# Optimization experiments

Measured on AMD Instinct MI355X. Metric: run time of the kernel, lower is better.

The kernel has to match this reference:

```python
import jax, jax.numpy as jnp
import numpy as np

K = 16
REP = 128
ASZ = 6
AENC = 64
BSK = 2048 * K  # bs*K flat batch


def _lin(k, fin, fout):
    return jax.random.normal(k, (fin, fout), jnp.float32) / np.float32(np.sqrt(fin))


def setup_inputs() -> dict:
    key = jax.random.key(0)
    ks = jax.random.split(key, 20)
    inp = {
        "lambda1": jax.random.normal(ks[0], (BSK, REP), jnp.float32),
        "actions": jax.random.normal(ks[1], (BSK, ASZ), jnp.float32),
    }
    # (fan_in, hidden, fan_out) per rlkit Mlp((hidden,), out, in)
    specs = {
        "le": (REP, REP, REP),            # lambda_encoder
        "ae": (ASZ, REP, AENC),           # action_encoder
        "aef": (AENC + REP, REP, REP),    # action_effect_network
        "aat": (AENC + REP, REP, 1),      # action_attention_network
        "pe": (2 * REP, 2 * REP, REP),    # pairwise_encoder_network
        "ie": (REP, REP, AENC),           # interaction_effect_network
        "ia": (REP, REP, 1),              # interaction_attention_network
        "fm": (AENC + REP, REP, REP),     # final_merge_network
    }
    i = 2
    for name, (fin, h, fout) in specs.items():
        inp[name + "_W1"] = _lin(ks[i], fin, h)
        inp[name + "_b1"] = jnp.zeros((h,), jnp.float32)
        inp[name + "_W2"] = _lin(ks[i + 1], h, fout)
        inp[name + "_b2"] = jnp.zeros((fout,), jnp.float32)
        i += 2
    return inp


def _mlp(x, W1, b1, W2, b2, out_act):
    h = jax.nn.elu(x @ W1 + b1)
    return out_act(h @ W2 + b2)


# constant all-pairs index lists (i != j), i-major as in the torch loop
_II = np.array([i for i in range(K) for j in range(K) if i != j])
_JJ = np.array([j for i in range(K) for j in range(K) if i != j])


def reference(lambda1, actions,
              le_W1, le_b1, le_W2, le_b2,
              ae_W1, ae_b1, ae_W2, ae_b2,
              aef_W1, aef_b1, aef_W2, aef_b2,
              aat_W1, aat_b1, aat_W2, aat_b2,
              pe_W1, pe_b1, pe_W2, pe_b2,
              ie_W1, ie_b1, ie_W2, ie_b2,
              ia_W1, ia_b1, ia_W2, ia_b2,
              fm_W1, fm_b1, fm_W2, fm_b2):
    elu, sig = jax.nn.elu, jax.nn.sigmoid
    ident = lambda z: z

    enc_flat = _mlp(lambda1, le_W1, le_b1, le_W2, le_b2, elu)        # (BSK, REP)
    a_enc = _mlp(actions, ae_W1, ae_b1, ae_W2, ae_b2, elu)           # (BSK, AENC)
    la = jnp.concatenate([enc_flat, a_enc], -1)                      # (BSK, REP+AENC)
    a_eff = _mlp(la, aef_W1, aef_b1, aef_W2, aef_b2, elu)            # (BSK, REP)
    a_att = _mlp(la, aat_W1, aat_b1, aat_W2, aat_b2, sig)            # (BSK, 1)
    enc = (a_eff * a_att).reshape(-1, K, REP)                        # (bs, K, REP)
    bs = enc.shape[0]

    # all ordered pairs (i, j), i != j -> concat sender/receiver states
    all_pairs = jnp.concatenate([enc[:, _II], enc[:, _JJ]], -1)      # (bs, K*(K-1), 2*REP)
    all_pairs = all_pairs.reshape(bs * K, K - 1, 2 * REP)

    pi = _mlp(all_pairs, pe_W1, pe_b1, pe_W2, pe_b2, elu)            # (bs*K, K-1, REP)
    effect = _mlp(pi, ie_W1, ie_b1, ie_W2, ie_b2, elu)               # (bs*K, K-1, AENC)
    attention = _mlp(pi, ia_W1, ia_b1, ia_W2, ia_b2, sig)            # (bs*K, K-1, 1)
    total_effect = (effect * attention).sum(1)                       # (bs*K, AENC)

    lam_eff = jnp.concatenate([enc_flat, total_effect], -1)          # (bs*K, REP+AENC)
    new_lambdas = _mlp(lam_eff, fm_W1, fm_b1, fm_W2, fm_b2, ident)   # (bs*K, REP)
    return new_lambdas
```

## Files before the change

kernel.cpp:

```cpp
#include <hip/hip_runtime.h>
#include <hip/hip_bf16.h>

typedef unsigned short ushort_t;
typedef unsigned int uint_t;
typedef short bf16x8 __attribute__((ext_vector_type(8)));
typedef float f32x4 __attribute__((ext_vector_type(4)));

#define MFMA16(a, b, c) __builtin_amdgcn_mfma_f32_16x16x32_bf16((a), (b), (c), 0, 0, 0)

__device__ __forceinline__ ushort_t f2bf(float f) {
  uint_t u = __float_as_uint(f);
  u += 0x7fffu + ((u >> 16) & 1u);
  return (ushort_t)(u >> 16);
}
__device__ __forceinline__ float bf2f(ushort_t h) {
  return __uint_as_float(((uint_t)h) << 16);
}
__device__ __forceinline__ uint_t pack2(float lo, float hi) {
  union { __hip_bfloat162 h; uint_t u; } cv;
  cv.h = __float22bfloat162_rn(float2{lo, hi});
  return cv.u;
}
__device__ __forceinline__ uint2 pack4(f32x4 v) {
  uint2 o;
  o.x = pack2(v[0], v[1]);
  o.y = pack2(v[2], v[3]);
  return o;
}
__device__ __forceinline__ float eluf(float x) {
  float e = __expf(x) - 1.0f;
  return x > 0.0f ? x : e;
}
__device__ __forceinline__ float sigmf(float x) {
  return 1.0f / (1.0f + __expf(-x));
}
__device__ __forceinline__ int lds_off(int row, int colb, int ccb) {
  return row * ccb + (colb ^ ((row & 7) << 4));
}

constexpr size_t OFF_ENCF = 0;
constexpr size_t OFF_ENC  = 4194304;
constexpr size_t OFF_TEFF = 8388608;
constexpr size_t OFF_FR   = 10485760;
constexpr size_t OFF_U    = 10772480;
constexpr size_t OFF_V    = 19161088;

constexpr int FR_LE_W1  = 0;
constexpr int FR_LE_W2  = 16384;
constexpr int FR_AE_W2  = 32768;
constexpr int FR_AEF_W1 = 40960;
constexpr int FR_AAT_W1 = 65536;
constexpr int FR_AEF_W2 = 90112;
constexpr int FR_PE_W1  = 106496;
constexpr int FR_PE_W2  = 172032;
constexpr int FR_IE_W1  = 204800;
constexpr int FR_IE_W2  = 221184;
constexpr int FR_IA_W1  = 229376;
constexpr int FR_FM_W1  = 245760;
constexpr int FR_FM_W2  = 270336;

struct PrepDesc { const float* src; ushort_t* dst; int K; int N; };
struct PrepArgs { PrepDesc d[13]; };

__global__ __launch_bounds__(256) void prep_kernel(PrepArgs a) {
  PrepDesc p = a.d[blockIdx.y];
  int idx = blockIdx.x * 256 + threadIdx.x;
  if (idx >= p.K * p.N) return;
  int e = idx & 7;
  int lane = (idx >> 3) & 63;
  int f = idx >> 9;
  int ksteps = p.K >> 5;
  int kstep = f % ksteps;
  int ntile = f / ksteps;
  int k = kstep * 32 + ((lane >> 4) << 3) + e;
  int n = ntile * 16 + (lane & 15);
  p.dst[idx] = f2bf(p.src[k * p.N + n]);
}


template <int MT, int NT, int KS, int KSTR = KS>
__device__ __forceinline__ void reg_gemm_t(const bf16x8 x[MT][KS],
                                           const ushort_t* __restrict__ wfrag,
                                           int ntile0, int lane, f32x4 acc[MT][NT]) {
  const f32x4 z = {0.f, 0.f, 0.f, 0.f};
#pragma unroll
  for (int nt = 0; nt < NT; ++nt) {
#pragma unroll
    for (int m = 0; m < MT; ++m) acc[m][nt] = z;
    const ushort_t* wf = wfrag + (size_t)((ntile0 + nt) * KSTR) * 512 + lane * 8;
#pragma unroll
    for (int ks = 0; ks < KS; ++ks) {
      bf16x8 wfr = *(const bf16x8*)(wf + ks * 512);
#pragma unroll
      for (int m = 0; m < MT; ++m) acc[m][nt] = MFMA16(wfr, x[m][ks], acc[m][nt]);
    }
  }
}

template <int MT, int KS>
__device__ __forceinline__ void lds_load_x(const ushort_t* __restrict__ Abase, int lane,
                                           bf16x8 x[MT][KS]) {
  const int r = lane & 15, q = lane >> 4;
#pragma unroll
  for (int m = 0; m < MT; ++m)
#pragma unroll
    for (int ks = 0; ks < KS; ++ks) {
      int row = m * 16 + r;
      x[m][ks] = *(const bf16x8*)((const char*)Abase + lds_off(row, ks * 64 + q * 16, KS * 64));
    }
}

template <int MT, int NT, int KS>
__device__ __forceinline__ void lds_gemm_t(const ushort_t* __restrict__ Abase,
                                           const ushort_t* __restrict__ wfrag,
                                           int ntile0, int lane, f32x4 acc[MT][NT]) {
  bf16x8 x[MT][KS];
  lds_load_x<MT, KS>(Abase, lane, x);
  reg_gemm_t<MT, NT, KS>(x, wfrag, ntile0, lane, acc);
}

template <int MT, int NT, bool ELU>
__device__ __forceinline__ void add_bias_act_t(f32x4 acc[MT][NT], const float* __restrict__ bias,
                                               int col0, int lane) {
  const int q = lane >> 4;
#pragma unroll
  for (int nt = 0; nt < NT; ++nt) {
    f32x4 bv = *(const f32x4*)(bias + col0 + nt * 16 + q * 4);
#pragma unroll
    for (int m = 0; m < MT; ++m)
#pragma unroll
      for (int k = 0; k < 4; ++k) {
        float v = acc[m][nt][k] + bv[k];
        acc[m][nt][k] = ELU ? eluf(v) : v;
      }
  }
}

template <int MT, int NT, int CCB>
__device__ __forceinline__ void store_lds_t(ushort_t* Dbase, int col0, int lane,
                                            const f32x4 acc[MT][NT]) {
  const int r = lane & 15, q = lane >> 4;
#pragma unroll
  for (int m = 0; m < MT; ++m) {
    const int row = m * 16 + r;
#pragma unroll
    for (int nt = 0; nt < NT; ++nt) {
      int colb = (col0 + nt * 16 + q * 4) * 2;
      *(uint2*)((char*)Dbase + lds_off(row, colb, CCB)) = pack4(acc[m][nt]);
    }
  }
}

template <int MT, int NT>
__device__ __forceinline__ void store_global_t(ushort_t* __restrict__ G, int row0, int ncols,
                                               int col0, int lane, const f32x4 acc[MT][NT]) {
  const int r = lane & 15, q = lane >> 4;
#pragma unroll
  for (int m = 0; m < MT; ++m)
#pragma unroll
    for (int nt = 0; nt < NT; ++nt)
      *(uint2*)(G + (size_t)(row0 + m * 16 + r) * ncols + col0 + nt * 16 + q * 4) =
          pack4(acc[m][nt]);
}

__global__ __launch_bounds__(256, 2) void enc_kernel(
    const float* __restrict__ lambda1, const float* __restrict__ actions,
    const float* __restrict__ le_b1, const float* __restrict__ le_b2,
    const float* __restrict__ ae_W1, const float* __restrict__ ae_b1,
    const float* __restrict__ ae_b2, const float* __restrict__ aef_b1,
    const float* __restrict__ aef_b2, const float* __restrict__ aat_b1,
    const float* __restrict__ aat_W2, const float* __restrict__ aat_b2,
    const ushort_t* __restrict__ fr, ushort_t* __restrict__ encf, ushort_t* __restrict__ enc) {
  __shared__ __align__(16) ushort_t bufA[64 * 128];
  __shared__ __align__(16) ushort_t bufB[64 * 128];
  __shared__ __align__(16) ushort_t la[64 * 192];
  __shared__ float att[64];

  const int t = threadIdx.x, lane = t & 63, w = t >> 6;
  const int r = lane & 15, q = lane >> 4;
  const int rows0 = blockIdx.x * 64;

  {
    const int row = t >> 2, c0 = (t & 3) * 32;
    const float4* src = (const float4*)(lambda1 + (size_t)(rows0 + row) * 128 + c0);
#pragma unroll
    for (int j = 0; j < 8; ++j) {
      float4 v = src[j];
      f32x4 vv = {v.x, v.y, v.z, v.w};
      *(uint2*)((char*)bufA + lds_off(row, (c0 + j * 4) * 2, 256)) = pack4(vv);
    }
  }
  __syncthreads();

  f32x4 acc2[4][2];
  lds_gemm_t<4, 2, 4>(bufA, fr + FR_LE_W1, w * 2, lane, acc2);
  add_bias_act_t<4, 2, true>(acc2, le_b1, w * 32, lane);
  store_lds_t<4, 2, 256>(bufB, w * 32, lane, acc2);
  __syncthreads();
  lds_gemm_t<4, 2, 4>(bufB, fr + FR_LE_W2, w * 2, lane, acc2);
  add_bias_act_t<4, 2, true>(acc2, le_b2, w * 32, lane);
  store_lds_t<4, 2, 384>(la, w * 32, lane, acc2);
  store_global_t<4, 2>(encf, rows0, 128, w * 32, lane, acc2);
  {
    const int row = t >> 2, c0 = (t & 3) * 32;
    float a6[6];
#pragma unroll
    for (int k2 = 0; k2 < 6; ++k2) a6[k2] = actions[(size_t)(rows0 + row) * 6 + k2];
#pragma unroll
    for (int j = 0; j < 16; ++j) {
      int c = c0 + j * 2;
      float s0 = ae_b1[c], s1 = ae_b1[c + 1];
#pragma unroll
      for (int k2 = 0; k2 < 6; ++k2) {
        s0 += a6[k2] * ae_W1[k2 * 128 + c];
        s1 += a6[k2] * ae_W1[k2 * 128 + c + 1];
      }
      *(uint_t*)((char*)bufA + lds_off(row, c * 2, 256)) = pack2(eluf(s0), eluf(s1));
    }
  }
  __syncthreads();
  {
    f32x4 acc1[4][1];
    lds_gemm_t<4, 1, 4>(bufA, fr + FR_AE_W2, w, lane, acc1);
    add_bias_act_t<4, 1, true>(acc1, ae_b2, w * 16, lane);
    store_lds_t<4, 1, 384>(la, 128 + w * 16, lane, acc1);
  }
  __syncthreads();
  {
    bf16x8 xla[4][6];
    lds_load_x<4, 6>(la, lane, xla);
    reg_gemm_t<4, 2, 6>(xla, fr + FR_AEF_W1, w * 2, lane, acc2);
    add_bias_act_t<4, 2, true>(acc2, aef_b1, w * 32, lane);
    store_lds_t<4, 2, 256>(bufA, w * 32, lane, acc2);
    reg_gemm_t<4, 2, 6>(xla, fr + FR_AAT_W1, w * 2, lane, acc2);
    add_bias_act_t<4, 2, true>(acc2, aat_b1, w * 32, lane);
    store_lds_t<4, 2, 256>(bufB, w * 32, lane, acc2);
  }
  __syncthreads();
  lds_gemm_t<4, 2, 4>(bufA, fr + FR_AEF_W2, w * 2, lane, acc2);
  add_bias_act_t<4, 2, true>(acc2, aef_b2, w * 32, lane);
  {
    const int row = t >> 2, s = t & 3;
    float sum = 0.f;
#pragma unroll
    for (int j = 0; j < 32; ++j) {
      int c = s * 32 + j;
      sum += bf2f(*(const ushort_t*)((const char*)bufB + lds_off(row, c * 2, 256))) * aat_W2[c];
    }
    sum += __shfl_xor(sum, 1);
    sum += __shfl_xor(sum, 2);
    if (s == 0) att[row] = sigmf(sum + aat_b2[0]);
  }
  __syncthreads();
#pragma unroll
  for (int mt = 0; mt < 4; ++mt) {
    float av = att[mt * 16 + r];
#pragma unroll
    for (int nt = 0; nt < 2; ++nt) {
      f32x4 sv = acc2[mt][nt];
      sv[0] *= av; sv[1] *= av; sv[2] *= av; sv[3] *= av;
      *(uint2*)(enc + (size_t)(rows0 + mt * 16 + r) * 128 + w * 32 + nt * 16 + q * 4) = pack4(sv);
    }
  }
}

__global__ __launch_bounds__(256, 2) void uv_kernel(const ushort_t* __restrict__ enc,
                                                    const ushort_t* __restrict__ fr,
                                                    ushort_t* __restrict__ U,
                                                    ushort_t* __restrict__ V) {
  const int t = threadIdx.x, lane = t & 63, w = t >> 6;
  const int r = lane & 15, q = lane >> 4;
  const int rows0 = blockIdx.x * 64;
  const int half = blockIdx.y;

  bf16x8 x[4][4];
#pragma unroll
  for (int m = 0; m < 4; ++m)
#pragma unroll
    for (int ks = 0; ks < 4; ++ks)
      x[m][ks] = *(const bf16x8*)(enc + (size_t)(rows0 + m * 16 + r) * 128 + ks * 32 + q * 8);

  f32x4 acc[4][4];
  reg_gemm_t<4, 4, 4, 8>(x, fr + FR_PE_W1 + half * 4 * 512, w * 4, lane, acc);
  store_global_t<4, 4>(half ? V : U, rows0, 256, w * 64, lane, acc);
}

__global__ __launch_bounds__(256, 4) void pair_kernel(
    const ushort_t* __restrict__ U, const ushort_t* __restrict__ V,
    const ushort_t* __restrict__ fr,
    const float* __restrict__ pe_b1, const float* __restrict__ pe_b2,
    const float* __restrict__ ie_b1, const float* __restrict__ ie_b2,
    const float* __restrict__ ia_b1, const float* __restrict__ ia_W2,
    const float* __restrict__ ia_b2, ushort_t* __restrict__ teff) {
  __shared__ __align__(16) ushort_t hid[32 * 256];
  __shared__ __align__(16) ushort_t bufPi[32 * 128];
  __shared__ float att[32];

  const int t = threadIdx.x, lane = t & 63, w = t >> 6;
  const int r = lane & 15, q = lane >> 4;
  const int orig = ((blockIdx.x & 7) << 11) + (blockIdx.x >> 3);
  const int g0 = orig * 2;
  const int b = g0 >> 4;

  {
    const int token = t >> 3, c0 = (t & 7) * 32;
    const int im = (g0 + (token >> 4)) & 15;
    const ushort_t* Ur = U + (size_t)(b * 16 + im) * 256 + c0;
    const ushort_t* Vr = V + (size_t)(b * 16 + (token & 15)) * 256 + c0;
    const float* bp = pe_b1 + c0;
#pragma unroll
    for (int j4 = 0; j4 < 4; ++j4) {
      bf16x8 uu = *(const bf16x8*)(Ur + j4 * 8);
      bf16x8 vv = *(const bf16x8*)(Vr + j4 * 8);
      f32x4 b0 = *(const f32x4*)(bp + j4 * 8);
      f32x4 b1 = *(const f32x4*)(bp + j4 * 8 + 4);
      float h[8];
#pragma unroll
      for (int e = 0; e < 8; ++e) {
        float bb = (e < 4) ? b0[e] : b1[e - 4];
        h[e] = eluf(bf2f((ushort_t)uu[e]) + bf2f((ushort_t)vv[e]) + bb);
      }
      uint4 pk;
      pk.x = pack2(h[0], h[1]); pk.y = pack2(h[2], h[3]);
      pk.z = pack2(h[4], h[5]); pk.w = pack2(h[6], h[7]);
      *(uint4*)((char*)hid + lds_off(token, (c0 + j4 * 8) * 2, 512)) = pk;
    }
  }
  __syncthreads();
  {
    f32x4 acc[2][2];
    lds_gemm_t<2, 2, 8>(hid, fr + FR_PE_W2, w * 2, lane, acc);
    add_bias_act_t<2, 2, true>(acc, pe_b2, w * 32, lane);
    store_lds_t<2, 2, 256>(bufPi, w * 32, lane, acc);
  }
  __syncthreads();
  {
    bf16x8 x2[2][4];
    lds_load_x<2, 4>(bufPi, lane, x2);
    f32x4 acc[2][2];
    reg_gemm_t<2, 2, 4>(x2, fr + FR_IE_W1, w * 2, lane, acc);
    add_bias_act_t<2, 2, true>(acc, ie_b1, w * 32, lane);
    store_lds_t<2, 2, 256>(hid, w * 32, lane, acc);
    reg_gemm_t<2, 2, 4>(x2, fr + FR_IA_W1, w * 2, lane, acc);
    add_bias_act_t<2, 2, true>(acc, ia_b1, w * 32, lane);
    store_lds_t<2, 2, 256>(hid + 32 * 128, w * 32, lane, acc);
  }
  __syncthreads();
  f32x4 eff[2][1];
  lds_gemm_t<2, 1, 4>(hid, fr + FR_IE_W2, w, lane, eff);
  add_bias_act_t<2, 1, true>(eff, ie_b2, w * 16, lane);
  {
    const int row = t >> 3, s = t & 7;
    const char* hia = (const char*)(hid + 32 * 128);
    float sum = 0.f;
#pragma unroll
    for (int j = 0; j < 16; ++j) {
      int c = s * 16 + j;
      sum += bf2f(*(const ushort_t*)(hia + lds_off(row, c * 2, 256))) * ia_W2[c];
    }
    sum += __shfl_xor(sum, 1);
    sum += __shfl_xor(sum, 2);
    sum += __shfl_xor(sum, 4);
    if (s == 0) att[row] = sigmf(sum + ia_b2[0]);
  }
  __syncthreads();
#pragma unroll
  for (int mt = 0; mt < 2; ++mt) {
    const int im = (g0 + mt) & 15;
    const float av = (r == im) ? 0.f : att[mt * 16 + r];
    float v0 = eff[mt][0][0] * av, v1 = eff[mt][0][1] * av;
    float v2 = eff[mt][0][2] * av, v3 = eff[mt][0][3] * av;
#pragma unroll
    for (int d = 1; d < 16; d <<= 1) {
      v0 += __shfl_xor(v0, d);
      v1 += __shfl_xor(v1, d);
      v2 += __shfl_xor(v2, d);
      v3 += __shfl_xor(v3, d);
    }
    if (r == 0) {
      uint2 p;
      p.x = pack2(v0, v1);
      p.y = pack2(v2, v3);
      *(uint2*)(teff + (size_t)(g0 + mt) * 64 + w * 16 + q * 4) = p;
    }
  }
}

__global__ __launch_bounds__(256, 2) void fm_kernel(
    const ushort_t* __restrict__ encf, const ushort_t* __restrict__ teff,
    const ushort_t* __restrict__ fr, const float* __restrict__ fm_b1,
    const float* __restrict__ fm_b2, float* __restrict__ out) {
  __shared__ __align__(16) ushort_t bufH[64 * 128];
  const int t = threadIdx.x, lane = t & 63, w = t >> 6;
  const int r = lane & 15, q = lane >> 4;
  const int rows0 = blockIdx.x * 64;

  bf16x8 x[4][6];
#pragma unroll
  for (int mt = 0; mt < 4; ++mt) {
    const size_t row = rows0 + mt * 16 + r;
#pragma unroll
    for (int ks = 0; ks < 6; ++ks) {
      x[mt][ks] = (ks < 4) ? *(const bf16x8*)(encf + row * 128 + ks * 32 + q * 8)
                           : *(const bf16x8*)(teff + row * 64 + (ks - 4) * 32 + q * 8);
    }
  }
  f32x4 acc[4][2];
  reg_gemm_t<4, 2, 6>(x, fr + FR_FM_W1, w * 2, lane, acc);
  add_bias_act_t<4, 2, true>(acc, fm_b1, w * 32, lane);
  store_lds_t<4, 2, 256>(bufH, w * 32, lane, acc);
  __syncthreads();
  lds_gemm_t<4, 2, 4>(bufH, fr + FR_FM_W2, w * 2, lane, acc);
  add_bias_act_t<4, 2, false>(acc, fm_b2, w * 32, lane);
#pragma unroll
  for (int mt = 0; mt < 4; ++mt)
#pragma unroll
    for (int nt = 0; nt < 2; ++nt)
      *(f32x4*)(out + (size_t)(rows0 + mt * 16 + r) * 128 + w * 32 + nt * 16 + q * 4) =
          acc[mt][nt];
}

extern "C" void kernel_launch(void* const* d_in, const int* in_sizes, int n_in,
                              void* d_out, int out_size, void* d_ws, size_t ws_size,
                              hipStream_t stream) {
  (void)in_sizes; (void)n_in; (void)out_size; (void)ws_size;
  const float* lambda1 = (const float*)d_in[0];
  const float* actions = (const float*)d_in[1];

  ushort_t* ws = (ushort_t*)d_ws;
  ushort_t* encf = ws + OFF_ENCF;
  ushort_t* enc  = ws + OFF_ENC;
  ushort_t* teff = ws + OFF_TEFF;
  ushort_t* fr   = ws + OFF_FR;
  ushort_t* U    = ws + OFF_U;
  ushort_t* V    = ws + OFF_V;

  PrepArgs pa;
  const int src_idx[13] = {2, 4, 8, 10, 14, 12, 18, 20, 22, 24, 26, 30, 32};
  const int foff[13] = {FR_LE_W1, FR_LE_W2, FR_AE_W2, FR_AEF_W1, FR_AAT_W1, FR_AEF_W2,
                        FR_PE_W1, FR_PE_W2, FR_IE_W1, FR_IE_W2, FR_IA_W1, FR_FM_W1, FR_FM_W2};
  const int Ks[13] = {128, 128, 128, 192, 192, 128, 256, 256, 128, 128, 128, 192, 128};
  const int Ns[13] = {128, 128, 64, 128, 128, 128, 256, 128, 128, 64, 128, 128, 128};
  for (int i = 0; i < 13; ++i) {
    pa.d[i].src = (const float*)d_in[src_idx[i]];
    pa.d[i].dst = fr + foff[i];
    pa.d[i].K = Ks[i];
    pa.d[i].N = Ns[i];
  }
  prep_kernel<<<dim3(256, 13), 256, 0, stream>>>(pa);

  enc_kernel<<<512, 256, 0, stream>>>(
      lambda1, actions,
      (const float*)d_in[3], (const float*)d_in[5],
      (const float*)d_in[6], (const float*)d_in[7],
      (const float*)d_in[9],
      (const float*)d_in[11], (const float*)d_in[13],
      (const float*)d_in[15], (const float*)d_in[16],
      (const float*)d_in[17],
      fr, encf, enc);

  uv_kernel<<<dim3(512, 2), 256, 0, stream>>>(enc, fr, U, V);

  pair_kernel<<<16384, 256, 0, stream>>>(
      U, V, fr,
      (const float*)d_in[19], (const float*)d_in[21],
      (const float*)d_in[23], (const float*)d_in[25],
      (const float*)d_in[27], (const float*)d_in[28],
      (const float*)d_in[29],
      teff);

  fm_kernel<<<512, 256, 0, stream>>>(encf, teff, fr,
                                     (const float*)d_in[31], (const float*)d_in[33],
                                     (float*)d_out);
}
```

Measured before the change: 392.1 us.

## Make pair_kernel wave-independent with register-resident MLP chain and shuffle transposes

The pair kernel is restructured so that each wavefront handles two receiver groups entirely in registers. The pairwise, interaction-effect and attention MLPs are chained through MFMA outputs, with lane-shuffle transposes turning accumulator fragments back into operand fragments. This removes all LDS buffers and block-level barriers, and cuts the grid from 16384 to 4096 blocks at launch bound 2. In exchange, register pressure rises, and every wave now streams the full weight fragments from global/L2, whereas before waves split the output columns.

```diff
diff --git a/kernel.cpp b/kernel.cpp
--- a/kernel.cpp
+++ b/kernel.cpp
@@ -163,6 +163,26 @@
           pack4(acc[m][nt]);
 }
 
+__device__ __forceinline__ void transpose_frags(const uint2 P[8], int lane, bf16x8 x[4]) {
+  const int q = lane >> 4;
+  const int srcA = ((q & 1) * 2) * 16 + (lane & 15);
+  const int srcB = srcA + 16;
+  const bool hiSel = (q >> 1) & 1;
+#pragma unroll
+  for (int ks = 0; ks < 4; ++ks) {
+    uint_t l0x = __shfl((int)P[2 * ks].x, srcA), l0y = __shfl((int)P[2 * ks].y, srcA);
+    uint_t l1x = __shfl((int)P[2 * ks + 1].x, srcA), l1y = __shfl((int)P[2 * ks + 1].y, srcA);
+    uint_t h0x = __shfl((int)P[2 * ks].x, srcB), h0y = __shfl((int)P[2 * ks].y, srcB);
+    uint_t h1x = __shfl((int)P[2 * ks + 1].x, srcB), h1y = __shfl((int)P[2 * ks + 1].y, srcB);
+    uint4 v;
+    v.x = hiSel ? l1x : l0x;
+    v.y = hiSel ? l1y : l0y;
+    v.z = hiSel ? h1x : h0x;
+    v.w = hiSel ? h1y : h0y;
+    x[ks] = *(bf16x8*)&v;
+  }
+}
+
 __global__ __launch_bounds__(256, 2) void enc_kernel(
     const float* __restrict__ lambda1, const float* __restrict__ actions,
     const float* __restrict__ le_b1, const float* __restrict__ le_b2,
@@ -285,103 +305,145 @@
   store_global_t<4, 4>(half ? V : U, rows0, 256, w * 64, lane, acc);
 }
 
-__global__ __launch_bounds__(256, 4) void pair_kernel(
+__global__ __launch_bounds__(256, 2) void pair_kernel(
     const ushort_t* __restrict__ U, const ushort_t* __restrict__ V,
     const ushort_t* __restrict__ fr,
     const float* __restrict__ pe_b1, const float* __restrict__ pe_b2,
     const float* __restrict__ ie_b1, const float* __restrict__ ie_b2,
     const float* __restrict__ ia_b1, const float* __restrict__ ia_W2,
     const float* __restrict__ ia_b2, ushort_t* __restrict__ teff) {
-  __shared__ __align__(16) ushort_t hid[32 * 256];
-  __shared__ __align__(16) ushort_t bufPi[32 * 128];
-  __shared__ float att[32];
-
   const int t = threadIdx.x, lane = t & 63, w = t >> 6;
   const int r = lane & 15, q = lane >> 4;
-  const int orig = ((blockIdx.x & 7) << 11) + (blockIdx.x >> 3);
-  const int g0 = orig * 2;
+  const int pid = blockIdx.x >> 1, hh = blockIdx.x & 1;
+  const int blk = ((pid & 7) * 256 + (pid >> 3)) * 2 + hh;
+  const int g0 = blk * 8 + w * 2;
   const int b = g0 >> 4;
 
+  bf16x8 hf[2][8];
   {
-    const int token = t >> 3, c0 = (t & 7) * 32;
-    const int im = (g0 + (token >> 4)) & 15;
-    const ushort_t* Ur = U + (size_t)(b * 16 + im) * 256 + c0;
-    const ushort_t* Vr = V + (size_t)(b * 16 + (token & 15)) * 256 + c0;
-    const float* bp = pe_b1 + c0;
-#pragma unroll
-    for (int j4 = 0; j4 < 4; ++j4) {
-      bf16x8 uu = *(const bf16x8*)(Ur + j4 * 8);
-      bf16x8 vv = *(const bf16x8*)(Vr + j4 * 8);
-      f32x4 b0 = *(const f32x4*)(bp + j4 * 8);
-      f32x4 b1 = *(const f32x4*)(bp + j4 * 8 + 4);
-      float h[8];
+    const ushort_t* Vrow = V + (size_t)(b * 16 + r) * 256;
+    const ushort_t* Ur0 = U + (size_t)(b * 16 + ((g0 + 0) & 15)) * 256;
+    const ushort_t* Ur1 = U + (size_t)(b * 16 + ((g0 + 1) & 15)) * 256;
+#pragma unroll
+    for (int ks = 0; ks < 8; ++ks) {
+      const int k0 = ks * 32 + q * 8;
+      bf16x8 vv = *(const bf16x8*)(Vrow + k0);
+      bf16x8 u0 = *(const bf16x8*)(Ur0 + k0);
+      bf16x8 u1 = *(const bf16x8*)(Ur1 + k0);
+      f32x4 b0 = *(const f32x4*)(pe_b1 + k0);
+      f32x4 b1 = *(const f32x4*)(pe_b1 + k0 + 4);
+      float h0[8], h1[8];
 #pragma unroll
       for (int e = 0; e < 8; ++e) {
-        float bb = (e < 4) ? b0[e] : b1[e - 4];
-        h[e] = eluf(bf2f((ushort_t)uu[e]) + bf2f((ushort_t)vv[e]) + bb);
+        float vb = bf2f((ushort_t)vv[e]) + ((e < 4) ? b0[e] : b1[e - 4]);
+        h0[e] = eluf(bf2f((ushort_t)u0[e]) + vb);
+        h1[e] = eluf(bf2f((ushort_t)u1[e]) + vb);
       }
-      uint4 pk;
-      pk.x = pack2(h[0], h[1]); pk.y = pack2(h[2], h[3]);
-      pk.z = pack2(h[4], h[5]); pk.w = pack2(h[6], h[7]);
-      *(uint4*)((char*)hid + lds_off(token, (c0 + j4 * 8) * 2, 512)) = pk;
-    }
-  }
-  __syncthreads();
-  {
-    f32x4 acc[2][2];
-    lds_gemm_t<2, 2, 8>(hid, fr + FR_PE_W2, w * 2, lane, acc);
-    add_bias_act_t<2, 2, true>(acc, pe_b2, w * 32, lane);
-    store_lds_t<2, 2, 256>(bufPi, w * 32, lane, acc);
-  }
-  __syncthreads();
-  {
-    bf16x8 x2[2][4];
-    lds_load_x<2, 4>(bufPi, lane, x2);
-    f32x4 acc[2][2];
-    reg_gemm_t<2, 2, 4>(x2, fr + FR_IE_W1, w * 2, lane, acc);
-    add_bias_act_t<2, 2, true>(acc, ie_b1, w * 32, lane);
-    store_lds_t<2, 2, 256>(hid, w * 32, lane, acc);
-    reg_gemm_t<2, 2, 4>(x2, fr + FR_IA_W1, w * 2, lane, acc);
-    add_bias_act_t<2, 2, true>(acc, ia_b1, w * 32, lane);
-    store_lds_t<2, 2, 256>(hid + 32 * 128, w * 32, lane, acc);
-  }
-  __syncthreads();
-  f32x4 eff[2][1];
-  lds_gemm_t<2, 1, 4>(hid, fr + FR_IE_W2, w, lane, eff);
-  add_bias_act_t<2, 1, true>(eff, ie_b2, w * 16, lane);
-  {
-    const int row = t >> 3, s = t & 7;
-    const char* hia = (const char*)(hid + 32 * 128);
-    float sum = 0.f;
-#pragma unroll
-    for (int j = 0; j < 16; ++j) {
-      int c = s * 16 + j;
-      sum += bf2f(*(const ushort_t*)(hia + lds_off(row, c * 2, 256))) * ia_W2[c];
-    }
-    sum += __shfl_xor(sum, 1);
-    sum += __shfl_xor(sum, 2);
-    sum += __shfl_xor(sum, 4);
-    if (s == 0) att[row] = sigmf(sum + ia_b2[0]);
-  }
-  __syncthreads();
-#pragma unroll
-  for (int mt = 0; mt < 2; ++mt) {
-    const int im = (g0 + mt) & 15;
-    const float av = (r == im) ? 0.f : att[mt * 16 + r];
-    float v0 = eff[mt][0][0] * av, v1 = eff[mt][0][1] * av;
-    float v2 = eff[mt][0][2] * av, v3 = eff[mt][0][3] * av;
+      uint4 p0, p1;
+      p0.x = pack2(h0[0], h0[1]); p0.y = pack2(h0[2], h0[3]);
+      p0.z = pack2(h0[4], h0[5]); p0.w = pack2(h0[6], h0[7]);
+      p1.x = pack2(h1[0], h1[1]); p1.y = pack2(h1[2], h1[3]);
+      p1.z = pack2(h1[4], h1[5]); p1.w = pack2(h1[6], h1[7]);
+      hf[0][ks] = *(bf16x8*)&p0;
+      hf[1][ks] = *(bf16x8*)&p1;
+    }
+  }
+
+  const f32x4 z = {0.f, 0.f, 0.f, 0.f};
+  uint2 P[2][8];
+#pragma unroll
+  for (int nt = 0; nt < 8; ++nt) {
+    f32x4 a0 = z, a1 = z;
+    const ushort_t* wf = fr + FR_PE_W2 + (size_t)(nt * 8) * 512 + lane * 8;
+#pragma unroll
+    for (int ks = 0; ks < 8; ++ks) {
+      bf16x8 wfr = *(const bf16x8*)(wf + ks * 512);
+      a0 = MFMA16(wfr, hf[0][ks], a0);
+      a1 = MFMA16(wfr, hf[1][ks], a1);
+    }
+    f32x4 bv = *(const f32x4*)(pe_b2 + nt * 16 + q * 4);
+#pragma unroll
+    for (int k = 0; k < 4; ++k) {
+      a0[k] = eluf(a0[k] + bv[k]);
+      a1[k] = eluf(a1[k] + bv[k]);
+    }
+    P[0][nt] = pack4(a0);
+    P[1][nt] = pack4(a1);
+  }
+
+  bf16x8 x1[2][4];
+  transpose_frags(P[0], lane, x1[0]);
+  transpose_frags(P[1], lane, x1[1]);
+
+  uint2 Pe[2][8];
+  float attp0 = 0.f, attp1 = 0.f;
+#pragma unroll
+  for (int nt = 0; nt < 8; ++nt) {
+    f32x4 a0 = z, a1 = z, c0 = z, c1 = z;
+    const ushort_t* wfe = fr + FR_IE_W1 + (size_t)(nt * 4) * 512 + lane * 8;
+    const ushort_t* wfa = fr + FR_IA_W1 + (size_t)(nt * 4) * 512 + lane * 8;
+#pragma unroll
+    for (int ks = 0; ks < 4; ++ks) {
+      bf16x8 we = *(const bf16x8*)(wfe + ks * 512);
+      bf16x8 wa = *(const bf16x8*)(wfa + ks * 512);
+      a0 = MFMA16(we, x1[0][ks], a0);
+      a1 = MFMA16(we, x1[1][ks], a1);
+      c0 = MFMA16(wa, x1[0][ks], c0);
+      c1 = MFMA16(wa, x1[1][ks], c1);
+    }
+    f32x4 be = *(const f32x4*)(ie_b1 + nt * 16 + q * 4);
+    f32x4 ba = *(const f32x4*)(ia_b1 + nt * 16 + q * 4);
+    f32x4 w2 = *(const f32x4*)(ia_W2 + nt * 16 + q * 4);
+#pragma unroll
+    for (int k = 0; k < 4; ++k) {
+      a0[k] = eluf(a0[k] + be[k]);
+      a1[k] = eluf(a1[k] + be[k]);
+      attp0 += eluf(c0[k] + ba[k]) * w2[k];
+      attp1 += eluf(c1[k] + ba[k]) * w2[k];
+    }
+    Pe[0][nt] = pack4(a0);
+    Pe[1][nt] = pack4(a1);
+  }
+  attp0 += __shfl_xor(attp0, 16); attp0 += __shfl_xor(attp0, 32);
+  attp1 += __shfl_xor(attp1, 16); attp1 += __shfl_xor(attp1, 32);
+  const float att0 = sigmf(attp0 + ia_b2[0]);
+  const float att1 = sigmf(attp1 + ia_b2[0]);
+
+  bf16x8 x2[2][4];
+  transpose_frags(Pe[0], lane, x2[0]);
+  transpose_frags(Pe[1], lane, x2[1]);
+
+  const float av0 = (r == ((g0 + 0) & 15)) ? 0.f : att0;
+  const float av1 = (r == ((g0 + 1) & 15)) ? 0.f : att1;
+#pragma unroll
+  for (int nt = 0; nt < 4; ++nt) {
+    f32x4 a0 = z, a1 = z;
+    const ushort_t* wf = fr + FR_IE_W2 + (size_t)(nt * 4) * 512 + lane * 8;
+#pragma unroll
+    for (int ks = 0; ks < 4; ++ks) {
+      bf16x8 wfr = *(const bf16x8*)(wf + ks * 512);
+      a0 = MFMA16(wfr, x2[0][ks], a0);
+      a1 = MFMA16(wfr, x2[1][ks], a1);
+    }
+    f32x4 bv = *(const f32x4*)(ie_b2 + nt * 16 + q * 4);
+#pragma unroll
+    for (int k = 0; k < 4; ++k) {
+      a0[k] = eluf(a0[k] + bv[k]) * av0;
+      a1[k] = eluf(a1[k] + bv[k]) * av1;
+    }
 #pragma unroll
     for (int d = 1; d < 16; d <<= 1) {
-      v0 += __shfl_xor(v0, d);
-      v1 += __shfl_xor(v1, d);
-      v2 += __shfl_xor(v2, d);
-      v3 += __shfl_xor(v3, d);
+#pragma unroll
+      for (int k = 0; k < 4; ++k) {
+        a0[k] += __shfl_xor(a0[k], d);
+        a1[k] += __shfl_xor(a1[k], d);
+      }
     }
     if (r == 0) {
-      uint2 p;
-      p.x = pack2(v0, v1);
-      p.y = pack2(v2, v3);
-      *(uint2*)(teff + (size_t)(g0 + mt) * 64 + w * 16 + q * 4) = p;
+      *(uint_t*)(teff + (size_t)(g0 + 0) * 64 + nt * 16 + q * 4) = pack2(a0[0], a0[1]);
+      *(uint_t*)(teff + (size_t)(g0 + 0) * 64 + nt * 16 + q * 4 + 2) = pack2(a0[2], a0[3]);
+      *(uint_t*)(teff + (size_t)(g0 + 1) * 64 + nt * 16 + q * 4) = pack2(a1[0], a1[1]);
+      *(uint_t*)(teff + (size_t)(g0 + 1) * 64 + nt * 16 + q * 4 + 2) = pack2(a1[2], a1[3]);
     }
   }
 }
@@ -461,7 +523,7 @@
 
   uv_kernel<<<dim3(512, 2), 256, 0, stream>>>(enc, fr, U, V);
 
-  pair_kernel<<<16384, 256, 0, stream>>>(
+  pair_kernel<<<4096, 256, 0, stream>>>(
       U, V, fr,
       (const float*)d_in[19], (const float*)d_in[21],
       (const float*)d_in[23], (const float*)d_in[25],
```

Result: faster. 356.4 us (-9.1%).
